# Kernel tuning notes

Measured on AMD Instinct MI355X. Metric: run time of the kernel, lower is better.

Reference implementation:

```python
import jax, jax.numpy as jnp
import numpy as np

B, C, D, H, W = 1, 32, 32, 128, 128


def setup_inputs() -> dict:
    key = jax.random.key(0)
    kx, kq, kk, kv, ko = jax.random.split(key, 5)
    s = 1.0 / np.sqrt(C)
    return {
        "x": jax.random.normal(kx, (B, C, D, H, W), dtype=jnp.float32),
        "Wq": jax.random.normal(kq, (C, C), dtype=jnp.float32) * s,
        "Wk": jax.random.normal(kk, (C, C), dtype=jnp.float32) * s,
        "Wv": jax.random.normal(kv, (C, C), dtype=jnp.float32) * s,
        "Wo": jax.random.normal(ko, (C, C), dtype=jnp.float32) * s,
    }


def reference(x, Wq, Wk, Wv, Wo):
    # x: [B, C, D, H, W]; multi-dimensional (axial) self-attention:
    # independent softmax-attention along each spatial axis, outputs summed.
    scale = jnp.asarray(x.shape[1], x.dtype) ** -0.5
    q = jnp.einsum("bcdhw,oc->bodhw", x, Wq)
    k = jnp.einsum("bcdhw,oc->bodhw", x, Wk)
    v = jnp.einsum("bcdhw,oc->bodhw", x, Wv)

    # attention along D axis: scores [B, H, W, D, D]
    ad = jax.nn.softmax(jnp.einsum("bcdhw,bcehw->bhwde", q, k) * scale, axis=-1)
    od = jnp.einsum("bhwde,bcehw->bcdhw", ad, v)

    # attention along H axis: scores [B, D, W, H, H]
    ah = jax.nn.softmax(jnp.einsum("bcdhw,bcdgw->bdwhg", q, k) * scale, axis=-1)
    oh = jnp.einsum("bdwhg,bcdgw->bcdhw", ah, v)

    # attention along W axis: scores [B, D, H, W, W]
    aw = jax.nn.softmax(jnp.einsum("bcdhw,bcdhu->bdhwu", q, k) * scale, axis=-1)
    ow = jnp.einsum("bdhwu,bcdhu->bcdhw", aw, v)

    out = jnp.einsum("bcdhw,oc->bodhw", od + oh + ow, Wo) + x  # residual
    return out
```

## Files before the change

### kernel.cpp

```cpp
#include <hip/hip_runtime.h>


#define C_ 32
#define D_ 32
#define H_ 128
#define W_ 128
#define SC (D_*H_*W_)
#define SD (H_*W_)
#define SH (W_)
#define SCALE 0.17677669529663687f

typedef __attribute__((ext_vector_type(8))) short short8;
typedef __attribute__((ext_vector_type(4))) short short4v;
typedef __attribute__((ext_vector_type(2))) short short2v;
typedef __attribute__((ext_vector_type(4))) float f32x4;

#define MFMA16(a,b,c) __builtin_amdgcn_mfma_f32_16x16x32_bf16(a,b,c,0,0,0)

__device__ __forceinline__ int xcd_swz(int bid, int nwg) {
    int chunk = nwg >> 3;
    return (bid & 7) * chunk + (bid >> 3);
}
__device__ __forceinline__ short bf16_trunc(float f) {
    return (short)(__float_as_uint(f) >> 16);
}
__device__ __forceinline__ short bf16_rtne(float f) {
    unsigned u = __float_as_uint(f);
    unsigned r = u + 0x7FFFu + ((u >> 16) & 1u);
    return (short)(r >> 16);
}
__device__ __forceinline__ float bf16_tof(short s) {
    return __uint_as_float(((unsigned)(unsigned short)s) << 16);
}
__device__ __forceinline__ short8 ld8_b64x2(const short* p) {
    short4v a = *(const short4v*)p;
    short4v b = *(const short4v*)(p + 4);
    short8 o;
    o[0]=a[0]; o[1]=a[1]; o[2]=a[2]; o[3]=a[3];
    o[4]=b[0]; o[5]=b[1]; o[6]=b[2]; o[7]=b[3];
    return o;
}

__global__ __launch_bounds__(256) void kinit_kernel(
        const float* __restrict__ Wq, const float* __restrict__ Wk,
        const float* __restrict__ Wv, const float* __restrict__ Wo,
        short* __restrict__ ws) {
    int o = blockIdx.x * 256 + threadIdx.x;
    int a = o >> 5, b = o & 31;
    float m = 0.f, p = 0.f;
    #pragma unroll
    for (int k = 0; k < 32; ++k) {
        m += Wq[k*32+a] * Wk[k*32+b];
        p += Wo[a*32+k] * Wv[k*32+b];
    }
    m *= SCALE;
    short mh = bf16_trunc(m);
    ws[o]        = mh;
    ws[1024 + o] = bf16_trunc(m - bf16_tof(mh));
    short ph = bf16_trunc(p);
    ws[2048 + o] = ph;
    ws[3072 + o] = bf16_trunc(p - bf16_tof(ph));
}

#define TT_STRIDE 40
#define XH_STRIDE 136
#define P_STRIDE  136
#define R_BYTES   36864

__device__ __forceinline__ void slice_engine(
        const float* Xf, const short8 mah[2], const short8 mal[2],
        short* Tt_h, short* Tt_l, short* P, short* Xh,
        f32x4 uacc[2][2])
{
    const int t = threadIdx.x;
    const int wv = t >> 6, l = t & 63, hi = l >> 4, r = l & 15;
    const int qb = wv * 32;

    short8 xh_[2], xl_[2];
    #pragma unroll
    for (int nt = 0; nt < 2; ++nt) {
        int u = qb + nt*16 + r;
        #pragma unroll
        for (int j = 0; j < 8; ++j) {
            float f = Xf[(hi*8 + j)*128 + u];
            short h = bf16_trunc(f);
            xh_[nt][j] = h; xl_[nt][j] = bf16_trunc(f - bf16_tof(h));
        }
    }

    f32x4 tacc[2][2] = {};
    #pragma unroll
    for (int nt = 0; nt < 2; ++nt) {
        #pragma unroll
        for (int mt = 0; mt < 2; ++mt) {
            tacc[mt][nt] = MFMA16(mah[mt], xh_[nt], tacc[mt][nt]);
            tacc[mt][nt] = MFMA16(mah[mt], xl_[nt], tacc[mt][nt]);
            tacc[mt][nt] = MFMA16(mal[mt], xh_[nt], tacc[mt][nt]);
        }
    }
    #pragma unroll
    for (int mt = 0; mt < 2; ++mt)
    #pragma unroll
    for (int nt = 0; nt < 2; ++nt) {
        int u = qb + nt*16 + r;
        #pragma unroll
        for (int rp = 0; rp < 2; ++rp) {
            int c0 = 16*mt + 4*hi + 2*rp;
            float f0 = tacc[mt][nt][2*rp], f1 = tacc[mt][nt][2*rp+1];
            short h0 = bf16_trunc(f0), h1 = bf16_trunc(f1);
            short2v vh; vh[0] = h0; vh[1] = h1;
            *(short2v*)&Tt_h[u*TT_STRIDE + c0] = vh;
            short2v vl; vl[0] = bf16_trunc(f0 - bf16_tof(h0));
            vl[1] = bf16_trunc(f1 - bf16_tof(h1));
            *(short2v*)&Tt_l[u*TT_STRIDE + c0] = vl;
        }
    }
    __syncthreads();

    f32x4 sacc[2][8] = {};
    #pragma unroll
    for (int nt = 0; nt < 8; ++nt) {
        short8 th = *(const short8*)&Tt_h[(nt*16 + r)*TT_STRIDE + hi*8];
        short8 tl = *(const short8*)&Tt_l[(nt*16 + r)*TT_STRIDE + hi*8];
        #pragma unroll
        for (int qt = 0; qt < 2; ++qt) {
            sacc[qt][nt] = MFMA16(xh_[qt], th, sacc[qt][nt]);
            sacc[qt][nt] = MFMA16(xh_[qt], tl, sacc[qt][nt]);
            sacc[qt][nt] = MFMA16(xl_[qt], th, sacc[qt][nt]);
        }
    }
    float rls[2][4];
    #pragma unroll
    for (int qt = 0; qt < 2; ++qt)
    #pragma unroll
    for (int reg = 0; reg < 4; ++reg) {
        float m = sacc[qt][0][reg];
        #pragma unroll
        for (int nt = 1; nt < 8; ++nt) m = fmaxf(m, sacc[qt][nt][reg]);
        m = fmaxf(m, __shfl_xor(m, 1));
        m = fmaxf(m, __shfl_xor(m, 2));
        m = fmaxf(m, __shfl_xor(m, 4));
        m = fmaxf(m, __shfl_xor(m, 8));
        float s = 0.f;
        #pragma unroll
        for (int nt = 0; nt < 8; ++nt) {
            float e = __expf(sacc[qt][nt][reg] - m);
            sacc[qt][nt][reg] = e; s += e;
        }
        s += __shfl_xor(s, 1);
        s += __shfl_xor(s, 2);
        s += __shfl_xor(s, 4);
        s += __shfl_xor(s, 8);
        rls[qt][reg] = 1.f / s;
    }
    __syncthreads();
    #pragma unroll
    for (int qt = 0; qt < 2; ++qt)
    #pragma unroll
    for (int reg = 0; reg < 4; ++reg) {
        int q = qb + 16*qt + 4*hi + reg;
        float rl = rls[qt][reg];
        #pragma unroll
        for (int nt = 0; nt < 8; ++nt)
            P[q*P_STRIDE + nt*16 + r] = bf16_rtne(sacc[qt][nt][reg] * rl);
    }
    __syncthreads();

    #pragma unroll
    for (int kt = 0; kt < 4; ++kt) {
        short8 xa[2], pb[2];
        #pragma unroll
        for (int mt = 0; mt < 2; ++mt)
            xa[mt] = *(const short8*)&Xh[(r + 16*mt)*XH_STRIDE + hi*8 + kt*32];
        #pragma unroll
        for (int nt = 0; nt < 2; ++nt)
            pb[nt] = *(const short8*)&P[(qb + 16*nt + r)*P_STRIDE + hi*8 + kt*32];
        #pragma unroll
        for (int mt = 0; mt < 2; ++mt)
        #pragma unroll
        for (int nt = 0; nt < 2; ++nt)
            uacc[mt][nt] = MFMA16(xa[mt], pb[nt], uacc[mt][nt]);
    }
}

__global__ __launch_bounds__(256) void kw_kernel(const float* __restrict__ x,
        const short* __restrict__ ws, float* __restrict__ U) {
    __shared__ __align__(16) char Rr[R_BYTES];
    __shared__ __align__(16) short Xh[32*XH_STRIDE];
    float* Xf = (float*)Rr;
    short* Tt_h = (short*)(Rr + 16384);
    short* Tt_l = (short*)(Rr + 26624);
    short* P = (short*)Rr;
    int bid = xcd_swz(blockIdx.x, gridDim.x);
    int d = bid >> 7, h = bid & 127;
    int t = threadIdx.x;
    const int wv = t >> 6, l = t & 63, hi = l >> 4, r = l & 15;
    short8 mah[2], mal[2];
    #pragma unroll
    for (int mt = 0; mt < 2; ++mt) {
        mah[mt] = *(const short8*)&ws[(r + 16*mt)*32 + hi*8];
        mal[mt] = *(const short8*)&ws[1024 + (r + 16*mt)*32 + hi*8];
    }
    const float* xs = x + d*SD + h*SH;
    #pragma unroll
    for (int k = 0; k < 4; ++k) {
        int idx = t + k*256;
        int c = idx >> 5, u4 = idx & 31;
        float4 v = *(const float4*)&xs[c*SC + u4*4];
        *(float4*)&Xf[c*128 + u4*4] = v;
        short4v hv;
        hv[0] = bf16_rtne(v.x); hv[1] = bf16_rtne(v.y);
        hv[2] = bf16_rtne(v.z); hv[3] = bf16_rtne(v.w);
        *(short4v*)&Xh[c*XH_STRIDE + u4*4] = hv;
    }
    __syncthreads();
    f32x4 uacc[2][2] = {};
    slice_engine(Xf, mah, mal, Tt_h, Tt_l, P, Xh, uacc);
    float* Uo = U + d*SD + h*SH;
    #pragma unroll
    for (int mt = 0; mt < 2; ++mt)
    #pragma unroll
    for (int nt = 0; nt < 2; ++nt)
    #pragma unroll
    for (int reg = 0; reg < 4; ++reg) {
        int c = 16*mt + 4*hi + reg;
        int q = wv*32 + 16*nt + r;
        Uo[c*SC + q] = uacc[mt][nt][reg];
    }
}

__global__ __launch_bounds__(256) void kh_kernel(const float* __restrict__ x,
        const short* __restrict__ ws, float* __restrict__ U) {
    __shared__ __align__(16) char Rr[R_BYTES];
    __shared__ __align__(16) short Xh[32*XH_STRIDE];
    float* Xf = (float*)Rr;
    short* Tt_h = (short*)(Rr + 16384);
    short* Tt_l = (short*)(Rr + 26624);
    short* P = (short*)Rr;
    int bid = xcd_swz(blockIdx.x, gridDim.x);
    int d = bid >> 7, w = bid & 127;
    int t = threadIdx.x;
    const int wv = t >> 6, l = t & 63, hi = l >> 4, r = l & 15;
    short8 mah[2], mal[2];
    #pragma unroll
    for (int mt = 0; mt < 2; ++mt) {
        mah[mt] = *(const short8*)&ws[(r + 16*mt)*32 + hi*8];
        mal[mt] = *(const short8*)&ws[1024 + (r + 16*mt)*32 + hi*8];
    }
    const float* xs = x + d*SD + w;
    #pragma unroll
    for (int k = 0; k < 16; ++k) {
        int idx = t + k*256;
        int c = idx >> 7, g = idx & 127;
        float f = xs[c*SC + g*SH];
        Xf[c*128 + g] = f;
        Xh[c*XH_STRIDE + g] = bf16_rtne(f);
    }
    __syncthreads();
    f32x4 uacc[2][2] = {};
    slice_engine(Xf, mah, mal, Tt_h, Tt_l, P, Xh, uacc);
    float* Uo = U + d*SD + w;
    #pragma unroll
    for (int mt = 0; mt < 2; ++mt)
    #pragma unroll
    for (int nt = 0; nt < 2; ++nt)
    #pragma unroll
    for (int reg = 0; reg < 4; ++reg) {
        int c = 16*mt + 4*hi + reg;
        int q = wv*32 + 16*nt + r;
        Uo[c*SC + q*SH] += uacc[mt][nt][reg];
    }
}

#define XJ 1152
#define KD_TTS 40
#define KD_PS  36
__global__ __launch_bounds__(256, 2) void kd_kernel(const float* __restrict__ x,
        const short* __restrict__ ws, float* __restrict__ UO) {
    __shared__ __align__(16) short Xh[8*XJ], Xl[8*XJ];
    __shared__ __align__(16) char Rr[33792];
    short* Tt_h = (short*)Rr;
    short* Tt_l = (short*)(Rr + 10240);
    short* Pp   = (short*)(Rr + 20480);
    float* u_lds = (float*)Rr;

    int bid = xcd_swz(blockIdx.x, gridDim.x);
    int h = bid >> 4, w0 = (bid & 15) * 8;
    int t = threadIdx.x;
    const int wv = t >> 6, l = t & 63, hi = l >> 4, r = l & 15;

    short8 mah[2], mal[2], pah[2], pal[2];
    #pragma unroll
    for (int mt = 0; mt < 2; ++mt) {
        mah[mt] = *(const short8*)&ws[(mt*16 + r)*32 + hi*8];
        mal[mt] = *(const short8*)&ws[1024 + (mt*16 + r)*32 + hi*8];
        pah[mt] = *(const short8*)&ws[2048 + (mt*16 + r)*32 + hi*8];
        pal[mt] = *(const short8*)&ws[3072 + (mt*16 + r)*32 + hi*8];
    }

    const float* xs = x + h*SH + w0;
    #pragma unroll
    for (int k = 0; k < 8; ++k) {
        int o = t + k*256;
        int j4 = o & 1, d = (o >> 1) & 31, c = o >> 6;
        float4 v = *(const float4*)(xs + c*SC + d*SD + j4*4);
        float fr[4] = {v.x, v.y, v.z, v.w};
        #pragma unroll
        for (int i = 0; i < 4; ++i) {
            short hh = bf16_trunc(fr[i]);
            Xh[((j4*4+i)*32 + c)*KD_PS + d] = hh;
            Xl[((j4*4+i)*32 + c)*KD_PS + d] = bf16_trunc(fr[i] - bf16_tof(hh));
        }
    }
    __syncthreads();

    f32x4 uacc[2][2][2] = {};
    float4 upre[8];

    #pragma unroll
    for (int ps = 0; ps < 2; ++ps) {
        int j = ps*4 + wv;
        const short* Xhj = &Xh[j*XJ];
        const short* Xlj = &Xl[j*XJ];
        short8 xph[2], xpl[2];
        #pragma unroll
        for (int et = 0; et < 2; ++et)
        #pragma unroll
        for (int jj = 0; jj < 8; ++jj) {
            int c = hi*8 + jj;
            xph[et][jj] = Xhj[c*KD_PS + et*16 + r];
            xpl[et][jj] = Xlj[c*KD_PS + et*16 + r];
        }
        f32x4 tacc[2][2] = {};
        #pragma unroll
        for (int et = 0; et < 2; ++et)
        #pragma unroll
        for (int mt = 0; mt < 2; ++mt) {
            tacc[mt][et] = MFMA16(mah[mt], xph[et], tacc[mt][et]);
            tacc[mt][et] = MFMA16(mah[mt], xpl[et], tacc[mt][et]);
            tacc[mt][et] = MFMA16(mal[mt], xph[et], tacc[mt][et]);
        }
        int tb = wv*32*KD_TTS;
        #pragma unroll
        for (int mt = 0; mt < 2; ++mt)
        #pragma unroll
        for (int et = 0; et < 2; ++et) {
            int e = et*16 + r;
            #pragma unroll
            for (int rp = 0; rp < 2; ++rp) {
                int c0 = mt*16 + hi*4 + rp*2;
                float f0 = tacc[mt][et][rp*2], f1 = tacc[mt][et][rp*2+1];
                short h0 = bf16_trunc(f0), h1 = bf16_trunc(f1);
                short2v vh; vh[0] = h0; vh[1] = h1;
                *(short2v*)&Tt_h[tb + e*KD_TTS + c0] = vh;
                short2v vl; vl[0] = bf16_trunc(f0 - bf16_tof(h0));
                vl[1] = bf16_trunc(f1 - bf16_tof(h1));
                *(short2v*)&Tt_l[tb + e*KD_TTS + c0] = vl;
            }
        }
        f32x4 sacc[2][2] = {};
        #pragma unroll
        for (int et = 0; et < 2; ++et) {
            short8 th = *(const short8*)&Tt_h[tb + (et*16 + r)*KD_TTS + hi*8];
            short8 tl = *(const short8*)&Tt_l[tb + (et*16 + r)*KD_TTS + hi*8];
            #pragma unroll
            for (int qt = 0; qt < 2; ++qt) {
                sacc[qt][et] = MFMA16(xph[qt], th, sacc[qt][et]);
                sacc[qt][et] = MFMA16(xph[qt], tl, sacc[qt][et]);
                sacc[qt][et] = MFMA16(xpl[qt], th, sacc[qt][et]);
            }
        }
        int pb = wv*32*KD_PS;
        #pragma unroll
        for (int qt = 0; qt < 2; ++qt)
        #pragma unroll
        for (int reg = 0; reg < 4; ++reg) {
            float m = fmaxf(sacc[qt][0][reg], sacc[qt][1][reg]);
            m = fmaxf(m, __shfl_xor(m, 1));
            m = fmaxf(m, __shfl_xor(m, 2));
            m = fmaxf(m, __shfl_xor(m, 4));
            m = fmaxf(m, __shfl_xor(m, 8));
            float e0 = __expf(sacc[qt][0][reg] - m);
            float e1 = __expf(sacc[qt][1][reg] - m);
            float s = e0 + e1;
            s += __shfl_xor(s, 1);
            s += __shfl_xor(s, 2);
            s += __shfl_xor(s, 4);
            s += __shfl_xor(s, 8);
            float rl = 1.f / s;
            int d = qt*16 + hi*4 + reg;
            Pp[pb + d*KD_PS + 0*16 + r] = bf16_rtne(e0 * rl);
            Pp[pb + d*KD_PS + 1*16 + r] = bf16_rtne(e1 * rl);
        }
        #pragma unroll
        for (int mt = 0; mt < 2; ++mt) {
            short8 xa = ld8_b64x2(&Xhj[(mt*16 + r)*KD_PS + hi*8]);
            #pragma unroll
            for (int nt = 0; nt < 2; ++nt) {
                short8 pbf = ld8_b64x2(&Pp[pb + (nt*16 + r)*KD_PS + hi*8]);
                uacc[ps][mt][nt] = MFMA16(xa, pbf, uacc[ps][mt][nt]);
            }
        }
        if (ps == 0) {
            #pragma unroll
            for (int k = 0; k < 8; ++k) {
                int o = t + k*256;
                int j4 = o & 1, d = (o >> 1) & 31, c = o >> 6;
                upre[k] = *(const float4*)(UO + c*SC + d*SD + h*SH + w0 + j4*4);
            }
        }
    }
    __syncthreads();
    #pragma unroll
    for (int k = 0; k < 8; ++k) {
        int o = t + k*256;
        int j4 = o & 1, d = (o >> 1) & 31, c = o >> 6;
        *(float4*)&u_lds[c*264 + d*8 + j4*4] = upre[k];
    }
    __syncthreads();
    #pragma unroll
    for (int ps = 0; ps < 2; ++ps)
    #pragma unroll
    for (int mt = 0; mt < 2; ++mt)
    #pragma unroll
    for (int nt = 0; nt < 2; ++nt)
    #pragma unroll
    for (int reg = 0; reg < 4; ++reg) {
        int c = mt*16 + hi*4 + reg;
        u_lds[c*264 + (nt*16 + r)*8 + ps*4 + wv] += uacc[ps][mt][nt][reg];
    }
    __syncthreads();
    f32x4 eacc[2][4] = {};
    #pragma unroll
    for (int nt = 0; nt < 4; ++nt) {
        short8 bh, bl;
        #pragma unroll
        for (int jj = 0; jj < 8; ++jj) {
            float f = u_lds[(hi*8 + jj)*264 + wv*64 + nt*16 + r];
            short hh = bf16_trunc(f);
            bh[jj] = hh; bl[jj] = bf16_trunc(f - bf16_tof(hh));
        }
        #pragma unroll
        for (int mt = 0; mt < 2; ++mt) {
            eacc[mt][nt] = MFMA16(pah[mt], bh, eacc[mt][nt]);
            eacc[mt][nt] = MFMA16(pah[mt], bl, eacc[mt][nt]);
            eacc[mt][nt] = MFMA16(pal[mt], bh, eacc[mt][nt]);
        }
    }
    #pragma unroll
    for (int mt = 0; mt < 2; ++mt)
    #pragma unroll
    for (int nt = 0; nt < 4; ++nt)
    #pragma unroll
    for (int reg = 0; reg < 4; ++reg) {
        int o = mt*16 + hi*4 + reg;
        int s = wv*64 + nt*16 + r;
        int addr = o*SC + (s >> 3)*SD + h*SH + w0 + (s & 7);
        UO[addr] = eacc[mt][nt][reg] + x[addr];
    }
}

extern "C" void kernel_launch(void* const* d_in, const int* in_sizes, int n_in,
                              void* d_out, int out_size, void* d_ws, size_t ws_size,
                              hipStream_t stream) {
    (void)in_sizes; (void)n_in; (void)out_size; (void)ws_size;
    const float* x  = (const float*)d_in[0];
    const float* Wq = (const float*)d_in[1];
    const float* Wk = (const float*)d_in[2];
    const float* Wv = (const float*)d_in[3];
    const float* Wo = (const float*)d_in[4];
    short* ws = (short*)d_ws;
    float* U = (float*)d_out;
    kinit_kernel<<<dim3(4), dim3(256), 0, stream>>>(Wq, Wk, Wv, Wo, ws);
    kw_kernel<<<dim3(4096), dim3(256), 0, stream>>>(x, ws, U);
    kh_kernel<<<dim3(4096), dim3(256), 0, stream>>>(x, ws, U);
    kd_kernel<<<dim3(2048), dim3(256), 0, stream>>>(x, ws, U);
}
```

Baseline: 430.7 us.

## Process two adjacent W columns per H-attention block with float2 loads

The H-axis attention kernel now handles two neighbouring w positions per block, loading x and updating U with float2 accesses instead of scalar strided accesses. The second column's fp32 slice is staged in an extra LDS buffer and run through the slice engine after the first. The aim is better coalescing on the strided global reads and read-modify-writes, and half as many blocks. The cost is extra LDS per block, which may reduce occupancy, plus serialised work within each block.

```diff
diff --git a/kernel.cpp b/kernel.cpp
--- a/kernel.cpp
+++ b/kernel.cpp
@@ -232,13 +232,14 @@
 __global__ __launch_bounds__(256) void kh_kernel(const float* __restrict__ x,
         const short* __restrict__ ws, float* __restrict__ U) {
     __shared__ __align__(16) char Rr[R_BYTES];
+    __shared__ __align__(16) float Xf1[32*128];
     __shared__ __align__(16) short Xh[32*XH_STRIDE];
-    float* Xf = (float*)Rr;
+    float* Xf0 = (float*)Rr;
     short* Tt_h = (short*)(Rr + 16384);
     short* Tt_l = (short*)(Rr + 26624);
     short* P = (short*)Rr;
     int bid = xcd_swz(blockIdx.x, gridDim.x);
-    int d = bid >> 7, w = bid & 127;
+    int d = bid >> 6, w0 = (bid & 63) * 2;
     int t = threadIdx.x;
     const int wv = t >> 6, l = t & 63, hi = l >> 4, r = l & 15;
     short8 mah[2], mal[2];
@@ -247,19 +248,30 @@
         mah[mt] = *(const short8*)&ws[(r + 16*mt)*32 + hi*8];
         mal[mt] = *(const short8*)&ws[1024 + (r + 16*mt)*32 + hi*8];
     }
-    const float* xs = x + d*SD + w;
+    const float* xs = x + d*SD + w0;
     #pragma unroll
     for (int k = 0; k < 16; ++k) {
         int idx = t + k*256;
         int c = idx >> 7, g = idx & 127;
-        float f = xs[c*SC + g*SH];
-        Xf[c*128 + g] = f;
-        Xh[c*XH_STRIDE + g] = bf16_rtne(f);
-    }
-    __syncthreads();
-    f32x4 uacc[2][2] = {};
-    slice_engine(Xf, mah, mal, Tt_h, Tt_l, P, Xh, uacc);
-    float* Uo = U + d*SD + w;
+        float2 v = *(const float2*)&xs[c*SC + g*SH];
+        Xf0[c*128+g] = v.x;
+        Xf1[c*128+g] = v.y;
+        Xh[c*XH_STRIDE+g] = bf16_rtne(v.x);
+    }
+    __syncthreads();
+    f32x4 u0[2][2] = {}, u1[2][2] = {};
+    slice_engine(Xf0, mah, mal, Tt_h, Tt_l, P, Xh, u0);
+    __syncthreads();
+    #pragma unroll
+    for (int k = 0; k < 8; ++k) {
+        int idx = t + k*256;
+        int g2 = idx & 63, c = idx >> 6;
+        float2 v = *(const float2*)&Xf1[c*128 + g2*2];
+        short2v hv; hv[0] = bf16_rtne(v.x); hv[1] = bf16_rtne(v.y);
+        *(short2v*)&Xh[c*XH_STRIDE + g2*2] = hv;
+    }
+    slice_engine(Xf1, mah, mal, Tt_h, Tt_l, P, Xh, u1);
+    float* Uo = U + d*SD + w0;
     #pragma unroll
     for (int mt = 0; mt < 2; ++mt)
     #pragma unroll
@@ -268,7 +280,11 @@
     for (int reg = 0; reg < 4; ++reg) {
         int c = 16*mt + 4*hi + reg;
         int q = wv*32 + 16*nt + r;
-        Uo[c*SC + q*SH] += uacc[mt][nt][reg];
+        float2* p = (float2*)&Uo[c*SC + q*SH];
+        float2 v = *p;
+        v.x += u0[mt][nt][reg];
+        v.y += u1[mt][nt][reg];
+        *p = v;
     }
 }
 
@@ -473,6 +489,6 @@
     float* U = (float*)d_out;
     kinit_kernel<<<dim3(4), dim3(256), 0, stream>>>(Wq, Wk, Wv, Wo, ws);
     kw_kernel<<<dim3(4096), dim3(256), 0, stream>>>(x, ws, U);
-    kh_kernel<<<dim3(4096), dim3(256), 0, stream>>>(x, ws, U);
+    kh_kernel<<<dim3(2048), dim3(256), 0, stream>>>(x, ws, U);
     kd_kernel<<<dim3(2048), dim3(256), 0, stream>>>(x, ws, U);
 }
```

New measurement: 348.7 us. 1.24x faster.
